# Kernel optimization log

Hardware: AMD Instinct MI355X
Metric: run time of the kernel (lower is better)

## Reference

```python
import jax, jax.numpy as jnp
import numpy as np

DIM = 128
HEADS = 4
POS_DIM = (DIM // 4) // 4  # DynamicPosBias: pos_dim = (dim//4)//4 = 8


def _layernorm(x, g, b, eps=1e-5):
    m = x.mean(-1, keepdims=True)
    v = x.var(-1, keepdims=True)
    return (x - m) / jnp.sqrt(v + eps) * g + b


def setup_inputs() -> dict:
    key = jax.random.key(0)
    ks = jax.random.split(key, 16)
    B_, N, C = 64, 512, DIM
    s = 0.02
    inp = {
        "x": jax.random.normal(ks[0], (B_, N, C), jnp.float32),
        "y": jax.random.normal(ks[1], (B_, N, C), jnp.float32),
        "H": 8, "W": 8, "D": 8,
        "qkv_w": jax.random.normal(ks[2], (3 * C, C), jnp.float32) * s,
        "qkv_b": jnp.zeros((3 * C,), jnp.float32),
        "proj_w": jax.random.normal(ks[3], (C, C), jnp.float32) * s,
        "proj_b": jnp.zeros((C,), jnp.float32),
        "pos_proj_w": jax.random.normal(ks[4], (POS_DIM, 3), jnp.float32) * s,
        "pos_proj_b": jnp.zeros((POS_DIM,), jnp.float32),
        "ln1_g": jnp.ones((POS_DIM,), jnp.float32),
        "ln1_b": jnp.zeros((POS_DIM,), jnp.float32),
        "p1_w": jax.random.normal(ks[5], (POS_DIM, POS_DIM), jnp.float32) * s,
        "p1_b": jnp.zeros((POS_DIM,), jnp.float32),
        "ln2_g": jnp.ones((POS_DIM,), jnp.float32),
        "ln2_b": jnp.zeros((POS_DIM,), jnp.float32),
        "p2_w": jax.random.normal(ks[6], (POS_DIM, POS_DIM), jnp.float32) * s,
        "p2_b": jnp.zeros((POS_DIM,), jnp.float32),
        "ln3_g": jnp.ones((POS_DIM,), jnp.float32),
        "ln3_b": jnp.zeros((POS_DIM,), jnp.float32),
        "p3_w": jax.random.normal(ks[7], (HEADS, POS_DIM), jnp.float32) * s,
        "p3_b": jnp.zeros((HEADS,), jnp.float32),
    }
    return inp


def _rel_pos_static(H, W, D):
    # biases table: all relative offsets, shape ((2H-1)(2W-1)(2D-1), 3)
    bh = np.arange(1 - H, H)
    bw = np.arange(1 - W, W)
    bd = np.arange(1 - D, D)
    biases = np.stack(np.meshgrid(bh, bw, bd, indexing="ij")).reshape(3, -1).T
    # relative position index, shape (N, N)
    coords = np.stack(np.meshgrid(np.arange(H), np.arange(W), np.arange(D), indexing="ij")).reshape(3, -1)
    rel = coords[:, :, None] - coords[:, None, :]  # (3, N, N)
    rel = rel.transpose(1, 2, 0).astype(np.int64)
    rel[:, :, 0] += H - 1
    rel[:, :, 1] += W - 1
    rel[:, :, 2] += D - 1
    rel[:, :, 0] *= (2 * W - 1) * (2 * D - 1)
    rel[:, :, 1] *= 2 * D - 1
    idx = rel.sum(-1)  # (N, N)
    return jnp.asarray(biases, jnp.float32), jnp.asarray(idx)


def reference(x, y, H, W, D, qkv_w, qkv_b, proj_w, proj_b,
              pos_proj_w, pos_proj_b, ln1_g, ln1_b, p1_w, p1_b,
              ln2_g, ln2_b, p2_w, p2_b, ln3_g, ln3_b, p3_w, p3_b):
    B_, N, C = x.shape
    h = p3_b.shape[0]
    hd = C // h
    scale = hd ** -0.5

    def qkv_fn(t):
        q3 = (t @ qkv_w.T + qkv_b).reshape(B_, N, 3, h, hd)
        q3 = q3.transpose(2, 0, 3, 1, 4)  # (3, B, h, N, hd)
        return q3[0], q3[1], q3[2]

    q, k, v = qkv_fn(x)
    # NOTE: original code uses self.qkv(y) (not qkv_y) -- reproduced faithfully
    q_y, k_y, v_y = qkv_fn(y)

    attn = jnp.einsum("bhnd,bhmd->bhnm", q * scale, k_y)  # (B, h, N, N)

    biases, idx = _rel_pos_static(H, W, D)
    # DynamicPosBias, residual=False: pos3(pos2(pos1(pos_proj(b))))
    pos = biases @ pos_proj_w.T + pos_proj_b
    pos = jax.nn.relu(_layernorm(pos, ln1_g, ln1_b)) @ p1_w.T + p1_b
    pos = jax.nn.relu(_layernorm(pos, ln2_g, ln2_b)) @ p2_w.T + p2_b
    pos = jax.nn.relu(_layernorm(pos, ln3_g, ln3_b)) @ p3_w.T + p3_b  # (table, h)
    rpb = pos[idx.reshape(-1)].reshape(N, N, h).transpose(2, 0, 1)  # (h, N, N)

    attn = jax.nn.softmax(attn + rpb[None], axis=-1)
    out = jnp.einsum("bhnm,bhmd->bhnd", attn, v_y)
    out = out.transpose(0, 2, 1, 3).reshape(B_, N, C)
    out = out @ proj_w.T + proj_b
    return out
```

## Files before the change

### kernel.cpp

```cpp
#include <hip/hip_runtime.h>
#include <hip/hip_bf16.h>

typedef __attribute__((ext_vector_type(4))) float f32x4;
typedef __attribute__((ext_vector_type(8))) short bf16x8;
typedef __attribute__((ext_vector_type(4))) short bf16x4;
typedef __attribute__((ext_vector_type(2))) unsigned int u32x2;

#define DEV static __device__ __forceinline__

constexpr float LOG2E  = 1.4426950408889634f;
constexpr float QSCALE = 0.17677669529663687f * LOG2E;

constexpr size_t OFF_Q   = 0;
constexpr size_t OFF_K   = (size_t)8  << 20;
constexpr size_t OFF_V   = (size_t)16 << 20;
constexpr size_t OFF_RPB = (size_t)24 << 20;
constexpr size_t OFF_AO  = (size_t)27 << 20;
constexpr size_t OFF_POS = (size_t)35 << 20;
constexpr size_t OFF_WQ  = (size_t)36 << 20;
constexpr size_t OFF_WP  = (size_t)37 << 20;

DEV short f2b(float f) {
  union { __bf16 h; short s; } u;
  u.h = (__bf16)f;
  return u.s;
}
DEV float b2f(unsigned int u) {
  union { unsigned int u; float f; } x; x.u = u; return x.f;
}
DEV unsigned int pkbf(float a, float b) {
  union { __bf16 h; unsigned short s; } ua, ub;
  ua.h = (__bf16)a; ub.h = (__bf16)b;
  return (unsigned int)ua.s | ((unsigned int)ub.s << 16);
}

DEV void ln_relu8(const float* v, const float* __restrict__ g,
                  const float* __restrict__ b, float* t) {
  float m = 0.f;
#pragma unroll
  for (int i = 0; i < 8; i++) m += v[i];
  m *= 0.125f;
  float var = 0.f;
#pragma unroll
  for (int i = 0; i < 8; i++) { float d = v[i] - m; var += d * d; }
  var *= 0.125f;
  float inv = 1.0f / sqrtf(var + 1e-5f);
#pragma unroll
  for (int i = 0; i < 8; i++) {
    float u = (v[i] - m) * inv * g[i] + b[i];
    t[i] = u > 0.f ? u : 0.f;
  }
}

DEV void mm8(const float* t, const float* __restrict__ w,
             const float* __restrict__ c, float* o) {
#pragma unroll
  for (int oo = 0; oo < 8; oo++) {
    float a = c[oo];
#pragma unroll
    for (int i = 0; i < 8; i++) a += t[i] * w[oo * 8 + i];
    o[oo] = a;
  }
}

__global__ void ca_posmlp(
    const float* __restrict__ pw, const float* __restrict__ pb,
    const float* __restrict__ g1, const float* __restrict__ b1,
    const float* __restrict__ w1, const float* __restrict__ c1,
    const float* __restrict__ g2, const float* __restrict__ b2,
    const float* __restrict__ w2, const float* __restrict__ c2,
    const float* __restrict__ g3, const float* __restrict__ b3,
    const float* __restrict__ w3, const float* __restrict__ c3,
    float* __restrict__ pos_out) {
  int r = blockIdx.x * 256 + threadIdx.x;
  if (r >= 3375) return;
  float x0 = (float)(r / 225 - 7);
  float x1 = (float)((r / 15) % 15 - 7);
  float x2 = (float)(r % 15 - 7);
  float v[8], t[8], u[8];
#pragma unroll
  for (int o = 0; o < 8; o++)
    v[o] = x0 * pw[o * 3] + x1 * pw[o * 3 + 1] + x2 * pw[o * 3 + 2] + pb[o];
  ln_relu8(v, g1, b1, t);
  mm8(t, w1, c1, u);
  ln_relu8(u, g2, b2, t);
  mm8(t, w2, c2, v);
  ln_relu8(v, g3, b3, t);
#pragma unroll
  for (int hh = 0; hh < 4; hh++) {
    float a = c3[hh];
#pragma unroll
    for (int i = 0; i < 8; i++) a += t[i] * w3[hh * 8 + i];
    pos_out[r * 4 + hh] = a * LOG2E;
  }
}

__global__ void ca_rpbw(const float* __restrict__ pos, short* __restrict__ rpbf,
                        const float* __restrict__ qkv_w, const float* __restrict__ proj_w,
                        short* __restrict__ wq, short* __restrict__ wp) {
  const int blk = blockIdx.x;
  if (blk >= 1024) {
    int i = (blk - 1024) * 256 + threadIdx.x;
    if (i < 49152) {
      float f = qkv_w[i];
      if (i < 16384) f *= QSCALE;
      wq[i] = f2b(f);
    } else {
      wp[i - 49152] = f2b(proj_w[i - 49152]);
    }
    return;
  }
  int gid = blk * 256 + threadIdx.x;
  int lane = gid & 63, jc = (gid >> 6) & 31, qg = (gid >> 11) & 31, hh = gid >> 16;
  int q = qg * 16 + (lane & 15);
  int j0 = jc * 16 + (lane >> 4) * 4;
  bf16x4 outv;
#pragma unroll
  for (int r = 0; r < 4; r++) {
    int j = j0 + r;
    int rh = (q >> 6) - (j >> 6) + 7;
    int rw = ((q >> 3) & 7) - ((j >> 3) & 7) + 7;
    int rd = (q & 7) - (j & 7) + 7;
    int idx = (rh * 15 + rw) * 15 + rd;
    outv[r] = f2b(pos[idx * 4 + hh]);
  }
  *(bf16x4*)(rpbf + (size_t)gid * 4) = outv;
}

__global__ __launch_bounds__(256) void ca_qkv(
    const float* __restrict__ x, const float* __restrict__ y,
    const short* __restrict__ wq, const float* __restrict__ qkv_b,
    short* __restrict__ gq, short* __restrict__ gk, short* __restrict__ gv) {
  __shared__ short lds[16384];
  const int z = blockIdx.y;
  const int t0 = blockIdx.x * 64;
  const int b_ = t0 >> 9;
  const int n0 = t0 & 511;
  const int tid = threadIdx.x;
  const float* __restrict__ in = (z == 0) ? x : y;
#pragma unroll
  for (int i = 0; i < 8; i++) {
    int flat = i * 1024 + tid * 4;
    f32x4 f = *(const f32x4*)(in + (size_t)t0 * 128 + flat);
    int row = flat >> 7, col = flat & 127;
    bf16x4 hv;
#pragma unroll
    for (int e = 0; e < 4; e++) hv[e] = f2b(f[e]);
    *(bf16x4*)(lds + row * 136 + col) = hv;
  }
  __syncthreads();
  const int w = tid >> 6, lane = tid & 63, lr = lane & 15, lg = lane >> 4;
  bf16x8 afrag[4];
  {
    const short* ap = lds + (w * 16 + lr) * 136 + lg * 8;
#pragma unroll
    for (int k4 = 0; k4 < 4; k4++) afrag[k4] = *(const bf16x8*)(ap + k4 * 32);
  }
  __syncthreads();

  if (z == 0) {
#pragma unroll
    for (int ct = 0; ct < 8; ct++) {
      const int col = ct * 16;
      float bias = qkv_b[col + lr] * QSCALE;
      f32x4 acc = {bias, bias, bias, bias};
      const short* bp = wq + (size_t)(col + lr) * 128 + lg * 8;
#pragma unroll
      for (int k4 = 0; k4 < 4; k4++) {
        bf16x8 bfr = *(const bf16x8*)(bp + k4 * 32);
        acc = __builtin_amdgcn_mfma_f32_16x16x32_bf16(afrag[k4], bfr, acc, 0, 0, 0);
      }
      const int d = (ct & 1) * 16 + lr;
      const int base = (w * 4 + (ct >> 1)) * 512 + 128 * (d >> 3) + (d & 7);
#pragma unroll
      for (int r = 0; r < 4; r++)
        lds[base + (lg * 4 + r) * 8] = f2b(acc[r]);
    }
  } else {
#pragma unroll
    for (int ct = 0; ct < 16; ct++) {
      const int col = 128 + ct * 16;
      float bias = qkv_b[col + lr];
      f32x4 acc = {bias, bias, bias, bias};
      const short* bp = wq + (size_t)(col + lr) * 128 + lg * 8;
#pragma unroll
      for (int k4 = 0; k4 < 4; k4++) {
        bf16x8 bfr = *(const bf16x8*)(bp + k4 * 32);
        acc = __builtin_amdgcn_mfma_f32_16x16x32_bf16(afrag[k4], bfr, acc, 0, 0, 0);
      }
      if (ct >= 8) {
        const int hv_ = (ct - 8) >> 1;
        const int dh = (ct - 8) & 1;
        const int base = 8192 + (((hv_ * 2 + (w >> 1)) * 2 + dh) * 512) + lane * 8 + (w & 1) * 4;
        *(unsigned int*)(lds + base)     = pkbf(acc[0], acc[1]);
        *(unsigned int*)(lds + base + 2) = pkbf(acc[2], acc[3]);
      } else {
        const int d = (ct & 1) * 16 + lr;
        const int base = (w * 4 + (ct >> 1)) * 512 + 128 * (d >> 3) + (d & 7);
#pragma unroll
        for (int r = 0; r < 4; r++)
          lds[base + (lg * 4 + r) * 8] = f2b(acc[r]);
      }
    }
  }
  __syncthreads();
  if (z == 0) {
#pragma unroll
    for (int kk = 0; kk < 4; kk++) {
      const int c = kk * 4 + w, hh = c & 3, tg = c >> 2;
      bf16x8 vd = *(const bf16x8*)(lds + c * 512 + lane * 8);
      *(bf16x8*)(gq + (((size_t)b_ * 4 + hh) * 32 + (n0 >> 4) + tg) * 512 + lane * 8) = vd;
    }
  } else {
#pragma unroll
    for (int kk = 0; kk < 4; kk++) {
      const int c = kk * 4 + w, hh = c & 3, tg = c >> 2;
      bf16x8 vd = *(const bf16x8*)(lds + c * 512 + lane * 8);
      *(bf16x8*)(gk + (((size_t)b_ * 4 + hh) * 32 + (n0 >> 4) + tg) * 512 + lane * 8) = vd;
    }
#pragma unroll
    for (int kk = 0; kk < 4; kk++) {
      const int c = kk * 4 + w, hh = c >> 2, ul = (c >> 1) & 1, dh = c & 1;
      bf16x8 vd = *(const bf16x8*)(lds + 8192 + c * 512 + lane * 8);
      *(bf16x8*)(gv + ((((size_t)b_ * 4 + hh) * 16 + (n0 >> 5) + ul) * 2 + dh) * 512 + lane * 8) = vd;
    }
  }
}

DEV void stage_kv(const short* kg, const short* vg, short* buf, int T, int w, int lane) {
#pragma unroll
  for (int i = 0; i < 4; i++) {
    const int c = w * 4 + i;
    const short* src;
    short* dst;
    if (c < 8) {
      src = kg + ((size_t)(T * 8 + c)) * 512 + lane * 8;
      dst = buf + c * 512;
    } else {
      src = vg + ((size_t)(T * 8 + c - 8)) * 512 + lane * 8;
      dst = buf + 4096 + (c - 8) * 512;
    }
    __builtin_amdgcn_global_load_lds((const __attribute__((address_space(1))) void*)src,
                                     (__attribute__((address_space(3))) void*)dst, 16, 0, 0);
  }
}

__global__ __launch_bounds__(256, 4) void ca_attn(
    const short* __restrict__ qfrag, const short* __restrict__ kfrag,
    const short* __restrict__ vfrag, const short* __restrict__ rpbf,
    short* __restrict__ aob) {
  __shared__ short kv[2][8192];
  const int bid = blockIdx.x;
  const int qt = bid >> 8, rem = bid & 255;
  const int b_ = rem >> 2, hh = rem & 3;
  const int bh = b_ * 4 + hh;
  const int tid = threadIdx.x;
  const int w = tid >> 6, lane = tid & 63, lg = lane >> 4;
  const int q0 = qt * 64 + w * 16, qg = (q0 >> 4);

  const short* kg = kfrag + (size_t)bh * 16384;
  const short* vg = vfrag + (size_t)bh * 16384;
  const bf16x8 qf = *(const bf16x8*)(qfrag + ((size_t)bh * 32 + qg) * 512 + lane * 8);
  const short* bp = rpbf + ((size_t)(hh * 32 + qg) << 13) + lane * 4;

  union PU { bf16x8 v; unsigned int u[4]; };
  PU ones;
  ones.u[0] = 0x3F803F80u; ones.u[1] = 0x3F803F80u;
  ones.u[2] = 0x3F803F80u; ones.u[3] = 0x3F803F80u;

  stage_kv(kg, vg, &kv[0][0], 0, w, lane);
  __syncthreads();

  f32x4 o0 = {0.f, 0.f, 0.f, 0.f}, o1 = {0.f, 0.f, 0.f, 0.f}, o2 = {0.f, 0.f, 0.f, 0.f};

  for (int T = 0; T < 4; T++) {
    const int cur = T & 1;
    if (T < 3) stage_kv(kg, vg, &kv[cur ^ 1][0], T + 1, w, lane);
    const short* kt = &kv[cur][0];
    const short* vt = &kv[cur][4096];

    u32x2 bw[8];
#pragma unroll
    for (int t = 0; t < 8; t++) bw[t] = *(const u32x2*)(bp + (size_t)(T * 8 + t) * 256);

#pragma unroll
    for (int uu = 0; uu < 4; uu++) {
      PU p;
#pragma unroll
      for (int half = 0; half < 2; half++) {
        const int t = uu * 2 + half;
        bf16x8 kf = *(const bf16x8*)(kt + t * 512 + lane * 8);
        f32x4 cin;
        cin[0] = b2f(bw[t].x << 16);
        cin[1] = b2f(bw[t].x & 0xFFFF0000u);
        cin[2] = b2f(bw[t].y << 16);
        cin[3] = b2f(bw[t].y & 0xFFFF0000u);
        f32x4 s = __builtin_amdgcn_mfma_f32_16x16x32_bf16(kf, qf, cin, 0, 0, 0);
        p.u[half * 2 + 0] = pkbf(__builtin_exp2f(s[0]), __builtin_exp2f(s[1]));
        p.u[half * 2 + 1] = pkbf(__builtin_exp2f(s[2]), __builtin_exp2f(s[3]));
      }
      bf16x8 vf0 = *(const bf16x8*)(vt + (uu * 2 + 0) * 512 + lane * 8);
      bf16x8 vf1 = *(const bf16x8*)(vt + (uu * 2 + 1) * 512 + lane * 8);
      o0 = __builtin_amdgcn_mfma_f32_16x16x32_bf16(p.v, vf0, o0, 0, 0, 0);
      o1 = __builtin_amdgcn_mfma_f32_16x16x32_bf16(p.v, vf1, o1, 0, 0, 0);
      o2 = __builtin_amdgcn_mfma_f32_16x16x32_bf16(p.v, ones.v, o2, 0, 0, 0);
    }
    if (T < 3) __syncthreads();
  }

  short* pt = &kv[0][w * 1024];
  const int lr = lane & 15;
#pragma unroll
  for (int r = 0; r < 4; r++) {
    float iv = 1.0f / o2[r];
    pt[(lg * 4 + r) * 40 + lr] = f2b(o0[r] * iv);
    pt[(lg * 4 + r) * 40 + 16 + lr] = f2b(o1[r] * iv);
  }
  asm volatile("s_waitcnt lgkmcnt(0)" ::: "memory");
  __builtin_amdgcn_sched_barrier(0);
  {
    const int qq = lane >> 2, pp = lane & 3;
    bf16x8 od = *(const bf16x8*)(pt + qq * 40 + pp * 8);
    *(bf16x8*)(aob + ((size_t)bh * 512 + q0 + qq) * 32 + pp * 8) = od;
  }
}

__global__ __launch_bounds__(256) void ca_proj(
    const short* __restrict__ aob, const short* __restrict__ wp,
    const float* __restrict__ proj_b, float* __restrict__ out) {
  __shared__ float plds[8448];
  const int t0 = blockIdx.x * 64;
  const int b_ = t0 >> 9, n0 = t0 & 511;
  const int tid = threadIdx.x;
  const int w = tid >> 6, lane = tid & 63, lr = lane & 15, lg = lane >> 4;
  bf16x8 afrag[4];
#pragma unroll
  for (int k4 = 0; k4 < 4; k4++)
    afrag[k4] = *(const bf16x8*)(aob + (((size_t)b_ * 4 + k4) * 512 + n0 + w * 16 + lr) * 32 + lg * 8);
  float* pt = plds + w * 2112;
#pragma unroll
  for (int ct = 0; ct < 8; ct++) {
    float bias = proj_b[ct * 16 + lr];
    f32x4 acc = {bias, bias, bias, bias};
    const short* bp = wp + (size_t)(ct * 16 + lr) * 128 + lg * 8;
#pragma unroll
    for (int k4 = 0; k4 < 4; k4++) {
      bf16x8 bfr = *(const bf16x8*)(bp + k4 * 32);
      acc = __builtin_amdgcn_mfma_f32_16x16x32_bf16(afrag[k4], bfr, acc, 0, 0, 0);
    }
#pragma unroll
    for (int r = 0; r < 4; r++)
      pt[(lg * 4 + r) * 132 + ct * 16 + lr] = acc[r];
  }
  asm volatile("s_waitcnt lgkmcnt(0)" ::: "memory");
  __builtin_amdgcn_sched_barrier(0);
#pragma unroll
  for (int i = 0; i < 8; i++) {
    int f = i * 256 + lane * 4;
    int row = f >> 7, col = f & 127;
    f32x4 v = *(const f32x4*)(pt + row * 132 + col);
    *(f32x4*)(out + (size_t)(t0 + w * 16) * 128 + f) = v;
  }
}

extern "C" void kernel_launch(void* const* d_in, const int* in_sizes, int n_in,
                              void* d_out, int out_size, void* d_ws, size_t ws_size,
                              hipStream_t stream) {
  const float* x      = (const float*)d_in[0];
  const float* y      = (const float*)d_in[1];
  const float* qkv_w  = (const float*)d_in[5];
  const float* qkv_b  = (const float*)d_in[6];
  const float* proj_w = (const float*)d_in[7];
  const float* proj_b = (const float*)d_in[8];
  const float* pos_w  = (const float*)d_in[9];
  const float* pos_b  = (const float*)d_in[10];
  const float* ln1g = (const float*)d_in[11];
  const float* ln1b = (const float*)d_in[12];
  const float* p1w  = (const float*)d_in[13];
  const float* p1b  = (const float*)d_in[14];
  const float* ln2g = (const float*)d_in[15];
  const float* ln2b = (const float*)d_in[16];
  const float* p2w  = (const float*)d_in[17];
  const float* p2b  = (const float*)d_in[18];
  const float* ln3g = (const float*)d_in[19];
  const float* ln3b = (const float*)d_in[20];
  const float* p3w  = (const float*)d_in[21];
  const float* p3b  = (const float*)d_in[22];
  float* out = (float*)d_out;

  char* ws = (char*)d_ws;
  short* gq    = (short*)(ws + OFF_Q);
  short* gk    = (short*)(ws + OFF_K);
  short* gv    = (short*)(ws + OFF_V);
  short* rpbf  = (short*)(ws + OFF_RPB);
  short* aob   = (short*)(ws + OFF_AO);
  float* posb  = (float*)(ws + OFF_POS);
  short* wq    = (short*)(ws + OFF_WQ);
  short* wp    = (short*)(ws + OFF_WP);

  ca_posmlp<<<14, 256, 0, stream>>>(pos_w, pos_b, ln1g, ln1b, p1w, p1b,
                                    ln2g, ln2b, p2w, p2b, ln3g, ln3b, p3w, p3b, posb);
  ca_rpbw<<<1280, 256, 0, stream>>>(posb, rpbf, qkv_w, proj_w, wq, wp);
  ca_qkv<<<dim3(512, 2), 256, 0, stream>>>(x, y, wq, qkv_b, gq, gk, gv);
  ca_attn<<<2048, 256, 0, stream>>>(gq, gk, gv, rpbf, aob);
  ca_proj<<<512, 256, 0, stream>>>(aob, wp, proj_b, out);
}
```

Measured before the change: 83.56 us.

## Fuse pos-MLP, bias table and QKV into one kernel; convert weights inline

Merges the position-MLP, relative-bias expansion and QKV projection into a single launch, with 256 blocks recomputing the small MLP table into LDS per head and then expanding the bias. The separate weight-conversion pass is removed: QKV and projection kernels now read fp32 weights and convert them to bf16 in registers before each MFMA. This cuts two launches and their intermediate global buffers, at the cost of redundant MLP recomputation in every bias block and extra fp32 weight loads and conversions inside the GEMM loops.

```diff
diff --git a/kernel.cpp b/kernel.cpp
--- a/kernel.cpp
+++ b/kernel.cpp
@@ -16,9 +16,6 @@
 constexpr size_t OFF_V   = (size_t)16 << 20;
 constexpr size_t OFF_RPB = (size_t)24 << 20;
 constexpr size_t OFF_AO  = (size_t)27 << 20;
-constexpr size_t OFF_POS = (size_t)35 << 20;
-constexpr size_t OFF_WQ  = (size_t)36 << 20;
-constexpr size_t OFF_WP  = (size_t)37 << 20;
 
 DEV short f2b(float f) {
   union { __bf16 h; short s; } u;
@@ -33,6 +30,13 @@
   ua.h = (__bf16)a; ub.h = (__bf16)b;
   return (unsigned int)ua.s | ((unsigned int)ub.s << 16);
 }
+DEV bf16x8 w8(const float* __restrict__ p, float s) {
+  f32x4 a = *(const f32x4*)p, b = *(const f32x4*)(p + 4);
+  bf16x8 r;
+  r[0] = f2b(a[0] * s); r[1] = f2b(a[1] * s); r[2] = f2b(a[2] * s); r[3] = f2b(a[3] * s);
+  r[4] = f2b(b[0] * s); r[5] = f2b(b[1] * s); r[6] = f2b(b[2] * s); r[7] = f2b(b[3] * s);
+  return r;
+}
 
 DEV void ln_relu8(const float* v, const float* __restrict__ g,
                   const float* __restrict__ b, float* t) {
@@ -63,80 +67,70 @@
   }
 }
 
-__global__ void ca_posmlp(
+__global__ __launch_bounds__(256) void ca_pre_qkv(
+    const float* __restrict__ x, const float* __restrict__ y,
+    const float* __restrict__ qkv_w, const float* __restrict__ qkv_b,
+    short* __restrict__ gq, short* __restrict__ gk, short* __restrict__ gv,
+    short* __restrict__ rpbf,
     const float* __restrict__ pw, const float* __restrict__ pb,
     const float* __restrict__ g1, const float* __restrict__ b1,
     const float* __restrict__ w1, const float* __restrict__ c1,
     const float* __restrict__ g2, const float* __restrict__ b2,
     const float* __restrict__ w2, const float* __restrict__ c2,
     const float* __restrict__ g3, const float* __restrict__ b3,
-    const float* __restrict__ w3, const float* __restrict__ c3,
-    float* __restrict__ pos_out) {
-  int r = blockIdx.x * 256 + threadIdx.x;
-  if (r >= 3375) return;
-  float x0 = (float)(r / 225 - 7);
-  float x1 = (float)((r / 15) % 15 - 7);
-  float x2 = (float)(r % 15 - 7);
-  float v[8], t[8], u[8];
-#pragma unroll
-  for (int o = 0; o < 8; o++)
-    v[o] = x0 * pw[o * 3] + x1 * pw[o * 3 + 1] + x2 * pw[o * 3 + 2] + pb[o];
-  ln_relu8(v, g1, b1, t);
-  mm8(t, w1, c1, u);
-  ln_relu8(u, g2, b2, t);
-  mm8(t, w2, c2, v);
-  ln_relu8(v, g3, b3, t);
-#pragma unroll
-  for (int hh = 0; hh < 4; hh++) {
-    float a = c3[hh];
-#pragma unroll
-    for (int i = 0; i < 8; i++) a += t[i] * w3[hh * 8 + i];
-    pos_out[r * 4 + hh] = a * LOG2E;
-  }
-}
-
-__global__ void ca_rpbw(const float* __restrict__ pos, short* __restrict__ rpbf,
-                        const float* __restrict__ qkv_w, const float* __restrict__ proj_w,
-                        short* __restrict__ wq, short* __restrict__ wp) {
+    const float* __restrict__ w3, const float* __restrict__ c3) {
+  __shared__ short lds[16384];
   const int blk = blockIdx.x;
-  if (blk >= 1024) {
-    int i = (blk - 1024) * 256 + threadIdx.x;
-    if (i < 49152) {
-      float f = qkv_w[i];
-      if (i < 16384) f *= QSCALE;
-      wq[i] = f2b(f);
-    } else {
-      wp[i - 49152] = f2b(proj_w[i - 49152]);
+  const int tid = threadIdx.x;
+
+  if (blk < 256) {
+    float* plds = (float*)lds;
+    const int hh = blk >> 6;
+    for (int r = tid; r < 3375; r += 256) {
+      float x0 = (float)(r / 225 - 7);
+      float x1 = (float)((r / 15) % 15 - 7);
+      float x2 = (float)(r % 15 - 7);
+      float v[8], t[8], u[8];
+#pragma unroll
+      for (int o = 0; o < 8; o++)
+        v[o] = x0 * pw[o * 3] + x1 * pw[o * 3 + 1] + x2 * pw[o * 3 + 2] + pb[o];
+      ln_relu8(v, g1, b1, t);
+      mm8(t, w1, c1, u);
+      ln_relu8(u, g2, b2, t);
+      mm8(t, w2, c2, v);
+      ln_relu8(v, g3, b3, t);
+      float a = c3[hh];
+#pragma unroll
+      for (int i = 0; i < 8; i++) a += t[i] * w3[hh * 8 + i];
+      plds[r] = a * LOG2E;
+    }
+    __syncthreads();
+#pragma unroll
+    for (int k = 0; k < 4; k++) {
+      int gid = (hh << 16) + (blk & 63) * 1024 + k * 256 + tid;
+      int lane = gid & 63, jc = (gid >> 6) & 31, qg = (gid >> 11) & 31;
+      int q = qg * 16 + (lane & 15);
+      int j0 = jc * 16 + (lane >> 4) * 4;
+      bf16x4 outv;
+#pragma unroll
+      for (int r = 0; r < 4; r++) {
+        int j = j0 + r;
+        int rh = (q >> 6) - (j >> 6) + 7;
+        int rw = ((q >> 3) & 7) - ((j >> 3) & 7) + 7;
+        int rd = (q & 7) - (j & 7) + 7;
+        int idx = (rh * 15 + rw) * 15 + rd;
+        outv[r] = f2b(plds[idx]);
+      }
+      *(bf16x4*)(rpbf + (size_t)gid * 4) = outv;
     }
     return;
   }
-  int gid = blk * 256 + threadIdx.x;
-  int lane = gid & 63, jc = (gid >> 6) & 31, qg = (gid >> 11) & 31, hh = gid >> 16;
-  int q = qg * 16 + (lane & 15);
-  int j0 = jc * 16 + (lane >> 4) * 4;
-  bf16x4 outv;
-#pragma unroll
-  for (int r = 0; r < 4; r++) {
-    int j = j0 + r;
-    int rh = (q >> 6) - (j >> 6) + 7;
-    int rw = ((q >> 3) & 7) - ((j >> 3) & 7) + 7;
-    int rd = (q & 7) - (j & 7) + 7;
-    int idx = (rh * 15 + rw) * 15 + rd;
-    outv[r] = f2b(pos[idx * 4 + hh]);
-  }
-  *(bf16x4*)(rpbf + (size_t)gid * 4) = outv;
-}
-
-__global__ __launch_bounds__(256) void ca_qkv(
-    const float* __restrict__ x, const float* __restrict__ y,
-    const short* __restrict__ wq, const float* __restrict__ qkv_b,
-    short* __restrict__ gq, short* __restrict__ gk, short* __restrict__ gv) {
-  __shared__ short lds[16384];
-  const int z = blockIdx.y;
-  const int t0 = blockIdx.x * 64;
+
+  const int z = (blk - 256) >> 9;
+  const int xb = (blk - 256) & 511;
+  const int t0 = xb * 64;
   const int b_ = t0 >> 9;
   const int n0 = t0 & 511;
-  const int tid = threadIdx.x;
   const float* __restrict__ in = (z == 0) ? x : y;
 #pragma unroll
   for (int i = 0; i < 8; i++) {
@@ -164,10 +158,10 @@
       const int col = ct * 16;
       float bias = qkv_b[col + lr] * QSCALE;
       f32x4 acc = {bias, bias, bias, bias};
-      const short* bp = wq + (size_t)(col + lr) * 128 + lg * 8;
+      const float* bp = qkv_w + (size_t)(col + lr) * 128 + lg * 8;
 #pragma unroll
       for (int k4 = 0; k4 < 4; k4++) {
-        bf16x8 bfr = *(const bf16x8*)(bp + k4 * 32);
+        bf16x8 bfr = w8(bp + k4 * 32, QSCALE);
         acc = __builtin_amdgcn_mfma_f32_16x16x32_bf16(afrag[k4], bfr, acc, 0, 0, 0);
       }
       const int d = (ct & 1) * 16 + lr;
@@ -182,10 +176,10 @@
       const int col = 128 + ct * 16;
       float bias = qkv_b[col + lr];
       f32x4 acc = {bias, bias, bias, bias};
-      const short* bp = wq + (size_t)(col + lr) * 128 + lg * 8;
+      const float* bp = qkv_w + (size_t)(col + lr) * 128 + lg * 8;
 #pragma unroll
       for (int k4 = 0; k4 < 4; k4++) {
-        bf16x8 bfr = *(const bf16x8*)(bp + k4 * 32);
+        bf16x8 bfr = w8(bp + k4 * 32, 1.0f);
         acc = __builtin_amdgcn_mfma_f32_16x16x32_bf16(afrag[k4], bfr, acc, 0, 0, 0);
       }
       if (ct >= 8) {
@@ -326,7 +320,7 @@
 }
 
 __global__ __launch_bounds__(256) void ca_proj(
-    const short* __restrict__ aob, const short* __restrict__ wp,
+    const short* __restrict__ aob, const float* __restrict__ proj_w,
     const float* __restrict__ proj_b, float* __restrict__ out) {
   __shared__ float plds[8448];
   const int t0 = blockIdx.x * 64;
@@ -342,10 +336,10 @@
   for (int ct = 0; ct < 8; ct++) {
     float bias = proj_b[ct * 16 + lr];
     f32x4 acc = {bias, bias, bias, bias};
-    const short* bp = wp + (size_t)(ct * 16 + lr) * 128 + lg * 8;
+    const float* bp = proj_w + (size_t)(ct * 16 + lr) * 128 + lg * 8;
 #pragma unroll
     for (int k4 = 0; k4 < 4; k4++) {
-      bf16x8 bfr = *(const bf16x8*)(bp + k4 * 32);
+      bf16x8 bfr = w8(bp + k4 * 32, 1.0f);
       acc = __builtin_amdgcn_mfma_f32_16x16x32_bf16(afrag[k4], bfr, acc, 0, 0, 0);
     }
 #pragma unroll
@@ -394,14 +388,10 @@
   short* gv    = (short*)(ws + OFF_V);
   short* rpbf  = (short*)(ws + OFF_RPB);
   short* aob   = (short*)(ws + OFF_AO);
-  float* posb  = (float*)(ws + OFF_POS);
-  short* wq    = (short*)(ws + OFF_WQ);
-  short* wp    = (short*)(ws + OFF_WP);
-
-  ca_posmlp<<<14, 256, 0, stream>>>(pos_w, pos_b, ln1g, ln1b, p1w, p1b,
-                                    ln2g, ln2b, p2w, p2b, ln3g, ln3b, p3w, p3b, posb);
-  ca_rpbw<<<1280, 256, 0, stream>>>(posb, rpbf, qkv_w, proj_w, wq, wp);
-  ca_qkv<<<dim3(512, 2), 256, 0, stream>>>(x, y, wq, qkv_b, gq, gk, gv);
+
+  ca_pre_qkv<<<1280, 256, 0, stream>>>(x, y, qkv_w, qkv_b, gq, gk, gv, rpbf,
+                                       pos_w, pos_b, ln1g, ln1b, p1w, p1b,
+                                       ln2g, ln2b, p2w, p2b, ln3g, ln3b, p3w, p3b);
   ca_attn<<<2048, 256, 0, stream>>>(gq, gk, gv, rpbf, aob);
-  ca_proj<<<512, 256, 0, stream>>>(aob, wp, proj_b, out);
-}
+  ca_proj<<<512, 256, 0, stream>>>(aob, proj_w, proj_b, out);
+}
```

Result: slower. 103.5 us (+23.9%).
